# Kernel optimization log

Measured on AMD Instinct MI355X. Metric: run time of the kernel, lower is better.

The kernel has to match this reference:

```python
import jax, jax.numpy as jnp
import numpy as np

B, T, D_MODEL = 2, 2048, 2048
N_HEADS, N_KV = 16, 8
HEAD_DIM = D_MODEL // N_HEADS  # 128
EPS = 1e-6


def rmsnorm(x, g):
    # qwen-compatible: compute in fp32, scale by learned weight
    xf = x.astype(jnp.float32)
    var = jnp.mean(xf * xf, axis=-1, keepdims=True)
    return (xf * jax.lax.rsqrt(var + EPS) * g).astype(x.dtype)


def apply_rope(x, cos, sin):
    # x: [b, h, t, d]; cos/sin: [t, d]
    d = x.shape[-1]
    x1, x2 = x[..., : d // 2], x[..., d // 2 :]
    rotated = jnp.concatenate([-x2, x1], axis=-1)
    return x * cos[None, None, :, :] + rotated * sin[None, None, :, :]


def setup_inputs() -> dict:
    key = jax.random.key(0)
    ks = jax.random.split(key, 8)
    x = jax.random.normal(ks[0], (B, T, D_MODEL), dtype=jnp.float32)
    # causal mask: True = masked out
    mask = jnp.triu(jnp.ones((T, T), dtype=bool), k=1)
    # rope tables
    inv_freq = 1.0 / (1e6 ** (np.arange(0, HEAD_DIM, 2, dtype=np.float32) / HEAD_DIM))
    angles = np.arange(T, dtype=np.float32)[:, None] * inv_freq[None, :]  # [T, d/2]
    angles = np.concatenate([angles, angles], axis=1)  # [T, d]
    cos = jnp.asarray(np.cos(angles), dtype=jnp.float32)
    sin = jnp.asarray(np.sin(angles), dtype=jnp.float32)
    s = 0.02
    Wq = jax.random.normal(ks[1], (D_MODEL, D_MODEL), dtype=jnp.float32) * s
    Wk = jax.random.normal(ks[2], (N_KV * HEAD_DIM, D_MODEL), dtype=jnp.float32) * s
    Wv = jax.random.normal(ks[3], (N_KV * HEAD_DIM, D_MODEL), dtype=jnp.float32) * s
    Wo = jax.random.normal(ks[4], (D_MODEL, D_MODEL), dtype=jnp.float32) * s
    bo = jnp.zeros((D_MODEL,), dtype=jnp.float32)
    gq = jnp.ones((HEAD_DIM,), dtype=jnp.float32)
    gk = jnp.ones((HEAD_DIM,), dtype=jnp.float32)
    return {"x": x, "mask": mask, "cos": cos, "sin": sin, "Wq": Wq, "Wk": Wk,
            "Wv": Wv, "Wo": Wo, "bo": bo, "gq": gq, "gk": gk}


def reference(x, mask, cos, sin, Wq, Wk, Wv, Wo, bo, gq, gk):
    b, t, _ = x.shape
    # projections
    q = (x @ Wq.T).reshape(b, t, N_HEADS, HEAD_DIM)
    q = rmsnorm(q, gq).transpose(0, 2, 1, 3)          # [b, H, t, d]
    q = apply_rope(q, cos[:t], sin[:t])
    k = (x @ Wk.T).reshape(b, t, N_KV, HEAD_DIM)
    k = rmsnorm(k, gk).transpose(0, 2, 1, 3)          # [b, G, t, d]
    k = apply_rope(k, cos[:t], sin[:t])
    v = (x @ Wv.T).reshape(b, t, N_KV, HEAD_DIM).transpose(0, 2, 1, 3)
    # GQA broadcast of KV heads
    rep = N_HEADS // N_KV
    k = jnp.repeat(k, rep, axis=1)                    # [b, H, t, d]
    v = jnp.repeat(v, rep, axis=1)
    scores = jnp.einsum("bhqd,bhkd->bhqk", q, k)
    scores = jnp.where(mask[:t, :t][None, None], -jnp.inf, scores)
    attn = jax.nn.softmax(scores / jnp.sqrt(jnp.float32(HEAD_DIM)), axis=-1)
    out = jnp.einsum("bhqk,bhkd->bqhd", attn, v).reshape(b, t, N_HEADS * HEAD_DIM)
    return out @ Wo.T + bo
```

## Files before the change

### kernel.cpp

```cpp
#include <hip/hip_runtime.h>
#include <stdint.h>

#define B_ 2
#define T_ 2048
#define DM 2048
#define NH 16
#define NKV 8
#define HD 128
#define NQKV 4096
#define SCALE_ 0.08838834764831845f
#define SC2_ 0.12753102765f

typedef float fx4 __attribute__((ext_vector_type(4)));
typedef __bf16 bfx8 __attribute__((ext_vector_type(8)));
typedef unsigned short u16;
typedef unsigned int u32;

typedef __attribute__((address_space(1))) const void gas_t;
typedef __attribute__((address_space(3))) void las_t;

__device__ __forceinline__ u16 f2bf(float f) {
  u32 u = __float_as_uint(f);
  u = (u + 0x7fffu + ((u >> 16) & 1u)) >> 16;
  return (u16)u;
}

__device__ __forceinline__ void stage16(const void* g, void* l) {
  __builtin_amdgcn_global_load_lds((gas_t*)(uintptr_t)g, (las_t*)(uintptr_t)l,
                                   16, 0, 0);
}

__global__ void k_cvt(const float* __restrict__ in, u16* __restrict__ out, int n) {
  int i = (blockIdx.x * blockDim.x + threadIdx.x) * 4;
  if (i + 3 < n) {
    float4 v = *(const float4*)(in + i);
    u32 w0 = (u32)f2bf(v.x) | ((u32)f2bf(v.y) << 16);
    u32 w1 = (u32)f2bf(v.z) | ((u32)f2bf(v.w) << 16);
    *(uint2*)(out + i) = make_uint2(w0, w1);
  }
}

template <bool OUT_F32>
__global__ __launch_bounds__(256, 2) void k_gemm(const u16* __restrict__ A,
                                                 const u16* __restrict__ Bm,
                                                 void* __restrict__ Cv,
                                                 const float* __restrict__ bias,
                                                 int M, int N, int K) {
  __shared__ __align__(16) u16 As[128 * 32];
  __shared__ __align__(16) u16 Bs[128 * 32];
  const int nbn = N >> 7;
  const int bm = blockIdx.x / nbn, bn = blockIdx.x % nbn;
  const int tid = threadIdx.x;
  const int w = tid >> 6, lane = tid & 63;
  const int wr = w >> 1, wc = w & 1;
  const int lr = lane & 15, lg = lane >> 4;
  const u16* Ab = A + (size_t)bm * 128 * K;
  const u16* Bb = Bm + (size_t)bn * 128 * K;
  const int srow = lane >> 2, skc = (lane & 3) * 8;

  fx4 zero4 = {0.f, 0.f, 0.f, 0.f};
  fx4 acc[4][4];
#pragma unroll
  for (int m = 0; m < 4; m++)
#pragma unroll
    for (int n = 0; n < 4; n++) acc[m][n] = zero4;

  for (int k0 = 0; k0 < K; k0 += 32) {
#pragma unroll
    for (int t = 0; t < 2; t++) {
      int s = w + t * 4;
      stage16(Ab + (size_t)(s * 16 + srow) * K + k0 + skc, As + s * 512 + lane * 8);
      stage16(Bb + (size_t)(s * 16 + srow) * K + k0 + skc, Bs + s * 512 + lane * 8);
    }
    __syncthreads();
    bfx8 af[4], bfr[4];
#pragma unroll
    for (int m = 0; m < 4; m++)
      af[m] = *(const bfx8*)(As + (wr * 64 + m * 16 + lr) * 32 + lg * 8);
#pragma unroll
    for (int n = 0; n < 4; n++)
      bfr[n] = *(const bfx8*)(Bs + (wc * 64 + n * 16 + lr) * 32 + lg * 8);
#pragma unroll
    for (int m = 0; m < 4; m++)
#pragma unroll
      for (int n = 0; n < 4; n++)
        acc[m][n] = __builtin_amdgcn_mfma_f32_16x16x32_bf16(af[m], bfr[n], acc[m][n], 0, 0, 0);
    __syncthreads();
  }

  const int r0 = bm * 128 + wr * 64, c0 = bn * 128 + wc * 64;
#pragma unroll
  for (int m = 0; m < 4; m++) {
#pragma unroll
    for (int n = 0; n < 4; n++) {
      int c = c0 + n * 16 + lr;
#pragma unroll
      for (int i = 0; i < 4; i++) {
        int r = r0 + m * 16 + lg * 4 + i;
        if (OUT_F32) {
          ((float*)Cv)[(size_t)r * N + c] = acc[m][n][i] + bias[c];
        } else {
          ((u16*)Cv)[(size_t)r * N + c] = f2bf(acc[m][n][i]);
        }
      }
    }
  }
}

__global__ __launch_bounds__(256) void k_qkpost(const u16* __restrict__ qkv,
                                                const float* __restrict__ cosp,
                                                const float* __restrict__ sinp,
                                                const float* __restrict__ gq,
                                                const float* __restrict__ gk,
                                                u16* __restrict__ Qo,
                                                u16* __restrict__ Ko) {
  int bi = blockIdx.x;
  int hh = bi % 24;
  int t64 = (bi / 24) % 32;
  int b = bi / 768;
  int tid = threadIdx.x;
  int j = tid >> 2, p = tid & 3;
  int t = t64 * 64 + j;
  bool isq = hh < 16;
  int colbase = isq ? hh * 128 : 2048 + (hh - 16) * 128;
  const u16* src = qkv + ((size_t)(b * T_ + t)) * NQKV + colbase + p * 32;

  float xv[32];
#pragma unroll
  for (int c = 0; c < 4; c++) {
    uint4 raw = *(const uint4*)(src + c * 8);
    u32 wd[4] = {raw.x, raw.y, raw.z, raw.w};
#pragma unroll
    for (int q2 = 0; q2 < 4; q2++) {
      xv[c * 8 + q2 * 2 + 0] = __uint_as_float(wd[q2] << 16);
      xv[c * 8 + q2 * 2 + 1] = __uint_as_float(wd[q2] & 0xffff0000u);
    }
  }
  float ss = 0.f;
#pragma unroll
  for (int i = 0; i < 32; i++) ss += xv[i] * xv[i];
  ss += __shfl_xor(ss, 1);
  ss += __shfl_xor(ss, 2);
  float rinv = rsqrtf(ss * (1.0f / 128.0f) + 1e-6f);
  const float* g = isq ? gq : gk;
  const float* cr = cosp + (size_t)t * 128 + p * 32;
  const float* sr = sinp + (size_t)t * 128 + p * 32;

  float ov[32];
#pragma unroll
  for (int i = 0; i < 32; i++) {
    float y = xv[i] * rinv * g[p * 32 + i];
    float oth = __shfl_xor(y, 2);
    float rot = (p < 2) ? -oth : oth;
    ov[i] = y * cr[i] + rot * sr[i];
  }

  uint4 pk[4];
#pragma unroll
  for (int c = 0; c < 4; c++) {
    u32 wd[4];
#pragma unroll
    for (int q2 = 0; q2 < 4; q2++)
      wd[q2] = (u32)f2bf(ov[c * 8 + q2 * 2]) | ((u32)f2bf(ov[c * 8 + q2 * 2 + 1]) << 16);
    pk[c] = make_uint4(wd[0], wd[1], wd[2], wd[3]);
  }

  if (isq) {
    u16* dst = Qo + (((size_t)(b * NH + hh)) * T_ + t) * HD + p * 32;
#pragma unroll
    for (int c = 0; c < 4; c++) *(uint4*)(dst + c * 8) = pk[c];
  } else {
    int hk = hh - 16;
    u16* dstrow = Ko + (((size_t)(b * NKV + hk)) * T_ + t) * HD;
#pragma unroll
    for (int c = 0; c < 4; c++) {
      int C = p * 4 + c;
      int Cs = C ^ (t & 7);
      *(uint4*)(dstrow + Cs * 8) = pk[c];
    }
  }
}

__global__ __launch_bounds__(256) void k_vtr(const u16* __restrict__ qkv,
                                             u16* __restrict__ vt) {
  __shared__ __align__(16) u16 sm[128 * 64];
  int bi = blockIdx.x;
  int hv = bi & 7;
  int t64 = (bi >> 3) & 31;
  int b = bi >> 8;
  int tid = threadIdx.x;
#pragma unroll
  for (int it = 0; it < 4; it++) {
    int idx = tid + it * 256;
    int tok = idx >> 4, c = idx & 15;
    uint4 raw = *(const uint4*)(qkv + ((size_t)(b * T_ + t64 * 64 + tok)) * NQKV +
                                3072 + hv * 128 + c * 8);
    u32 wd[4] = {raw.x, raw.y, raw.z, raw.w};
#pragma unroll
    for (int q2 = 0; q2 < 4; q2++) {
      sm[(c * 8 + q2 * 2 + 0) * 64 + tok] = (u16)(wd[q2] & 0xffffu);
      sm[(c * 8 + q2 * 2 + 1) * 64 + tok] = (u16)(wd[q2] >> 16);
    }
  }
  __syncthreads();
  int d = tid >> 1, half = tid & 1;
  size_t rowb = (((size_t)(b * NKV + hv)) * HD + d) * T_ + t64 * 64;
#pragma unroll
  for (int c = 0; c < 4; c++) {
    int cg = half * 4 + c;
    int cs = cg ^ (d & 7);
    u32 wd[4];
#pragma unroll
    for (int q2 = 0; q2 < 4; q2++) {
      u32 lo = sm[d * 64 + half * 32 + c * 8 + 2 * q2];
      u32 hi = sm[d * 64 + half * 32 + c * 8 + 2 * q2 + 1];
      wd[q2] = lo | (hi << 16);
    }
    *(uint4*)(vt + rowb + cs * 8) = make_uint4(wd[0], wd[1], wd[2], wd[3]);
  }
}

__global__ __launch_bounds__(256, 2) void k_attn(const u16* __restrict__ Qg,
                                                 const u16* __restrict__ Kg,
                                                 const u16* __restrict__ Vg,
                                                 u16* __restrict__ Og) {
  __shared__ __align__(16) u16 Ks[2][64 * 128];
  __shared__ __align__(16) u16 Vs[2][128 * 64];
  __shared__ __align__(16) u16 Ps[4][16 * 64];
  const int bi = blockIdx.x;
  const int z = bi & 15, h = (bi >> 4) & 15, b = bi >> 8;
  const int hkv = h >> 1;
  const int tid = threadIdx.x, w = tid >> 6, lane = tid & 63;
  const int lr = lane & 15, lg = lane >> 4;
  const u16* kb = Kg + ((size_t)(b * NKV + hkv)) * T_ * HD;
  const u16* vb = Vg + ((size_t)(b * NKV + hkv)) * HD * T_;
  u16* pw = &Ps[w][0];
  const fx4 zero4 = {0.f, 0.f, 0.f, 0.f};

  int cur = 0;
  auto stageKV = [&](int buf, int kv0) {
    u16* Kd = &Ks[buf][0];
    u16* Vd = &Vs[buf][0];
#pragma unroll
    for (int it = 0; it < 4; it++) {
      int r = it * 16 + (tid >> 4);
      stage16(kb + (size_t)(kv0 + r) * HD + (tid & 15) * 8, Kd + it * 2048 + tid * 8);
      int d = it * 32 + (tid >> 3);
      stage16(vb + (size_t)d * T_ + kv0 + (tid & 7) * 8, Vd + it * 2048 + tid * 8);
    }
  };

#pragma unroll 1
  for (int hf = 0; hf < 2; hf++) {
    const int zt = hf ? (31 - z) : z;
    const int qr0 = zt * 64 + w * 16;
    const u16* qbase = Qg + (((size_t)(b * NH + h)) * T_ + qr0 + lr) * HD;
    bfx8 qf[4];
#pragma unroll
    for (int kk = 0; kk < 4; kk++) qf[kk] = *(const bfx8*)(qbase + kk * 32 + lg * 8);

    fx4 o[8];
#pragma unroll
    for (int nf = 0; nf < 8; nf++) o[nf] = zero4;
    float m_i[4] = {-1e30f, -1e30f, -1e30f, -1e30f};
    float l_i[4] = {0.f, 0.f, 0.f, 0.f};
    const int nch = zt + 1;

    stageKV(cur, 0);
    __syncthreads();

#pragma unroll 1
    for (int ch = 0; ch < nch; ch++) {
      if (ch + 1 < nch) stageKV(cur ^ 1, (ch + 1) * 64);
      const u16* Kd = &Ks[cur][0];
      const u16* Vd = &Vs[cur][0];
      const int kv0 = ch * 64;

      fx4 sa[4];
#pragma unroll
      for (int n = 0; n < 4; n++) sa[n] = zero4;
      __builtin_amdgcn_s_setprio(1);
#pragma unroll
      for (int n = 0; n < 4; n++) {
        const int kvl = n * 16 + lr;
        const u16* krow = Kd + kvl * 128;
#pragma unroll
        for (int kk = 0; kk < 4; kk++) {
          int cs = (kk * 4 + lg) ^ (kvl & 7);
          bfx8 kf = *(const bfx8*)(krow + cs * 8);
          sa[n] = __builtin_amdgcn_mfma_f32_16x16x32_bf16(qf[kk], kf, sa[n], 0, 0, 0);
        }
      }
      __builtin_amdgcn_s_setprio(0);

      float pv[4][4];
      if (ch == zt) {
#pragma unroll
        for (int n = 0; n < 4; n++) {
          int kcol = kv0 + n * 16 + lr;
#pragma unroll
          for (int i = 0; i < 4; i++) {
            int r = qr0 + 4 * lg + i;
            pv[n][i] = (kcol > r) ? -1e30f : sa[n][i] * SC2_;
          }
        }
      } else {
#pragma unroll
        for (int n = 0; n < 4; n++)
#pragma unroll
          for (int i = 0; i < 4; i++) pv[n][i] = sa[n][i] * SC2_;
      }

      float mx[4];
      bool need = false;
#pragma unroll
      for (int i = 0; i < 4; i++) {
        float m = fmaxf(fmaxf(pv[0][i], pv[1][i]), fmaxf(pv[2][i], pv[3][i]));
        m = fmaxf(m, __shfl_xor(m, 1));
        m = fmaxf(m, __shfl_xor(m, 2));
        m = fmaxf(m, __shfl_xor(m, 4));
        m = fmaxf(m, __shfl_xor(m, 8));
        mx[i] = m;
        need = need || (m > m_i[i] + 8.0f);
      }
      if (__any(need)) {
#pragma unroll
        for (int i = 0; i < 4; i++) {
          float mn = fmaxf(m_i[i], mx[i]);
          float f = exp2f(m_i[i] - mn);
          m_i[i] = mn;
          l_i[i] *= f;
#pragma unroll
          for (int nf = 0; nf < 8; nf++) o[nf][i] *= f;
        }
      }

#pragma unroll
      for (int i = 0; i < 4; i++) {
        int q = 4 * lg + i;
        u16* prow = pw + q * 64;
#pragma unroll
        for (int n = 0; n < 4; n++) {
          float p = exp2f(pv[n][i] - m_i[i]);
          l_i[i] += p;
          int chn = ((n * 2 + (lr >> 3)) ^ (q & 7));
          prow[chn * 8 + (lr & 7)] = f2bf(p);
        }
      }
      asm volatile("s_waitcnt lgkmcnt(0)" ::: "memory");

      bfx8 pa[2];
#pragma unroll
      for (int ks = 0; ks < 2; ks++) {
        int cp = (4 * ks + lg) ^ (lr & 7);
        pa[ks] = *(const bfx8*)(pw + lr * 64 + cp * 8);
      }
      __builtin_amdgcn_s_setprio(1);
#pragma unroll
      for (int nf = 0; nf < 8; nf++) {
        int d = nf * 16 + lr;
        const u16* vrow = Vd + d * 64;
#pragma unroll
        for (int ks = 0; ks < 2; ks++) {
          int cv = (4 * ks + lg) ^ (d & 7);
          bfx8 vf = *(const bfx8*)(vrow + cv * 8);
          o[nf] = __builtin_amdgcn_mfma_f32_16x16x32_bf16(pa[ks], vf, o[nf], 0, 0, 0);
        }
      }
      __builtin_amdgcn_s_setprio(0);
      __syncthreads();
      cur ^= 1;
    }

    float inv[4];
#pragma unroll
    for (int i = 0; i < 4; i++) {
      float l = l_i[i];
      l += __shfl_xor(l, 1);
      l += __shfl_xor(l, 2);
      l += __shfl_xor(l, 4);
      l += __shfl_xor(l, 8);
      inv[i] = 1.0f / l;
    }
    u16* ob = Og + ((size_t)(b * T_ + qr0)) * DM + h * HD;
#pragma unroll
    for (int nf = 0; nf < 8; nf++)
#pragma unroll
      for (int i = 0; i < 4; i++)
        ob[(size_t)(4 * lg + i) * DM + nf * 16 + lr] = f2bf(o[nf][i] * inv[i]);
  }
}

extern "C" void kernel_launch(void* const* d_in, const int* in_sizes, int n_in,
                              void* d_out, int out_size, void* d_ws, size_t ws_size,
                              hipStream_t stream) {
  const float* x = (const float*)d_in[0];
  const float* cosp = (const float*)d_in[2];
  const float* sinp = (const float*)d_in[3];
  const float* Wq = (const float*)d_in[4];
  const float* Wk = (const float*)d_in[5];
  const float* Wv = (const float*)d_in[6];
  const float* Wo = (const float*)d_in[7];
  const float* bo = (const float*)d_in[8];
  const float* gq = (const float*)d_in[9];
  const float* gk = (const float*)d_in[10];

  char* ws = (char*)d_ws;
  u16* xbf  = (u16*)(ws + 0);
  u16* wqkv = (u16*)(ws + 16777216);
  u16* wo   = (u16*)(ws + 33554432);
  u16* qkv  = (u16*)(ws + 41943040);
  u16* qb   = (u16*)(ws + 75497472);
  u16* kb   = (u16*)(ws + 92274688);
  u16* vt   = (u16*)(ws + 100663296);
  u16* ab   = (u16*)(ws + 109051904);
  float* out = (float*)d_out;

  k_cvt<<<8192, 256, 0, stream>>>(x, xbf, 8388608);
  k_cvt<<<4096, 256, 0, stream>>>(Wq, wqkv, 4194304);
  k_cvt<<<2048, 256, 0, stream>>>(Wk, wqkv + 4194304, 2097152);
  k_cvt<<<2048, 256, 0, stream>>>(Wv, wqkv + 6291456, 2097152);
  k_cvt<<<4096, 256, 0, stream>>>(Wo, wo, 4194304);

  k_gemm<false><<<1024, 256, 0, stream>>>(xbf, wqkv, qkv, nullptr, 4096, 4096, 2048);
  k_qkpost<<<1536, 256, 0, stream>>>(qkv, cosp, sinp, gq, gk, qb, kb);
  k_vtr<<<512, 256, 0, stream>>>(qkv, vt);
  k_attn<<<512, 256, 0, stream>>>(qb, kb, vt, ab);
  k_gemm<true><<<512, 256, 0, stream>>>(ab, wo, out, bo, 4096, 2048, 2048);
}
```

Before: 274.6 us.

## Add 256x256-tile pipelined GEMM for the QKV projection

Adds a new bf16 GEMM kernel with 256x256 output tiles, 512 threads, a double-buffered split-K LDS pipeline fed by direct global-to-LDS loads, swizzled LDS layout and raised wave priority around MFMA bursts. It replaces the 128x128 GEMM used for the fused QKV projection. The larger tile is meant to raise data reuse per loaded byte, and the interleaved staging to hide load latency. In exchange the grid drops to 256 blocks, roughly one per CU, and register pressure is high.

```diff
diff --git a/kernel.cpp b/kernel.cpp
--- a/kernel.cpp
+++ b/kernel.cpp
@@ -37,6 +37,142 @@
     u32 w0 = (u32)f2bf(v.x) | ((u32)f2bf(v.y) << 16);
     u32 w1 = (u32)f2bf(v.z) | ((u32)f2bf(v.w) << 16);
     *(uint2*)(out + i) = make_uint2(w0, w1);
+  }
+}
+
+__global__ __launch_bounds__(512, 2) void k_gemm256(const u16* __restrict__ A,
+                                                    const u16* __restrict__ Bm,
+                                                    u16* __restrict__ C,
+                                                    int M, int N, int K) {
+  __shared__ __align__(16) u16 As[2][2][256 * 32];
+  __shared__ __align__(16) u16 Bs[2][2][256 * 32];
+  const int nbn = N >> 8;
+  const int bm = blockIdx.x / nbn, bn = blockIdx.x % nbn;
+  const int tid = threadIdx.x;
+  const int w = tid >> 6, lane = tid & 63;
+  const int wm = w >> 2, wn = w & 3;
+  const int lr = lane & 15, lg = lane >> 4;
+  const int cw = (lg ^ ((lr >> 1) & 3)) * 8;
+  const u16* Ab = A + (size_t)bm * 256 * K;
+  const u16* Bb = Bm + (size_t)bn * 256 * K;
+  const int NT = K >> 6;
+
+  auto stage = [&](const u16* gb, u16* region, int tile, int kh) {
+#pragma unroll
+    for (int i = 0; i < 2; i++) {
+      int q = tid + i * 512;
+      int row = q >> 2, ch = q & 3;
+      int sc = ch ^ ((row >> 1) & 3);
+      stage16(gb + (size_t)row * K + tile * 64 + kh * 32 + sc * 8, region + q * 8);
+    }
+  };
+
+  fx4 acc[8][4];
+  const fx4 zero4 = {0.f, 0.f, 0.f, 0.f};
+#pragma unroll
+  for (int m = 0; m < 8; m++)
+#pragma unroll
+    for (int n = 0; n < 4; n++) acc[m][n] = zero4;
+
+  stage(Ab, &As[0][0][0], 0, 0);
+  stage(Bb, &Bs[0][0][0], 0, 0);
+  stage(Ab, &As[0][1][0], 0, 1);
+  stage(Bb, &Bs[0][1][0], 0, 1);
+  stage(Ab, &As[1][0][0], 1, 0);
+  stage(Bb, &Bs[1][0][0], 1, 0);
+  asm volatile("s_waitcnt vmcnt(4)" ::: "memory");
+  __builtin_amdgcn_s_barrier();
+
+  const int arow = (wm * 128 + lr) * 32;
+  const int brow = (wn * 64 + lr) * 32;
+  bfx8 af[4], bf[4];
+
+#pragma unroll 1
+  for (int t = 0; t < NT; t++) {
+    const u16* A0 = &As[t & 1][0][0];
+    const u16* A1 = &As[t & 1][1][0];
+    const u16* B0 = &Bs[t & 1][0][0];
+    const u16* B1 = &Bs[t & 1][1][0];
+    const int p1 = (t + 1) & 1, p2 = t & 1;
+
+#pragma unroll
+    for (int mi = 0; mi < 4; mi++) af[mi] = *(const bfx8*)(A0 + arow + mi * 512 + cw);
+#pragma unroll
+    for (int n = 0; n < 4; n++) bf[n] = *(const bfx8*)(B0 + brow + n * 512 + cw);
+    if (t + 1 < NT) stage(Ab, &As[p1][1][0], t + 1, 1);
+    __builtin_amdgcn_s_barrier();
+    asm volatile("s_waitcnt lgkmcnt(0)" ::: "memory");
+    __builtin_amdgcn_sched_barrier(0);
+    __builtin_amdgcn_s_setprio(1);
+#pragma unroll
+    for (int mi = 0; mi < 4; mi++)
+#pragma unroll
+      for (int n = 0; n < 4; n++)
+        acc[mi][n] = __builtin_amdgcn_mfma_f32_16x16x32_bf16(af[mi], bf[n], acc[mi][n], 0, 0, 0);
+    __builtin_amdgcn_s_setprio(0);
+    __builtin_amdgcn_s_barrier();
+
+#pragma unroll
+    for (int mi = 0; mi < 4; mi++)
+      af[mi] = *(const bfx8*)(A0 + arow + 2048 + mi * 512 + cw);
+    if (t + 1 < NT) stage(Bb, &Bs[p1][1][0], t + 1, 1);
+    __builtin_amdgcn_s_barrier();
+    asm volatile("s_waitcnt lgkmcnt(0)" ::: "memory");
+    __builtin_amdgcn_sched_barrier(0);
+    __builtin_amdgcn_s_setprio(1);
+#pragma unroll
+    for (int mi = 0; mi < 4; mi++)
+#pragma unroll
+      for (int n = 0; n < 4; n++)
+        acc[4 + mi][n] = __builtin_amdgcn_mfma_f32_16x16x32_bf16(af[mi], bf[n], acc[4 + mi][n], 0, 0, 0);
+    __builtin_amdgcn_s_setprio(0);
+    __builtin_amdgcn_s_barrier();
+
+#pragma unroll
+    for (int mi = 0; mi < 4; mi++) af[mi] = *(const bfx8*)(A1 + arow + mi * 512 + cw);
+#pragma unroll
+    for (int n = 0; n < 4; n++) bf[n] = *(const bfx8*)(B1 + brow + n * 512 + cw);
+    if (t + 2 < NT) stage(Ab, &As[p2][0][0], t + 2, 0);
+    __builtin_amdgcn_s_barrier();
+    asm volatile("s_waitcnt lgkmcnt(0)" ::: "memory");
+    __builtin_amdgcn_sched_barrier(0);
+    __builtin_amdgcn_s_setprio(1);
+#pragma unroll
+    for (int mi = 0; mi < 4; mi++)
+#pragma unroll
+      for (int n = 0; n < 4; n++)
+        acc[mi][n] = __builtin_amdgcn_mfma_f32_16x16x32_bf16(af[mi], bf[n], acc[mi][n], 0, 0, 0);
+    __builtin_amdgcn_s_setprio(0);
+    __builtin_amdgcn_s_barrier();
+
+#pragma unroll
+    for (int mi = 0; mi < 4; mi++)
+      af[mi] = *(const bfx8*)(A1 + arow + 2048 + mi * 512 + cw);
+    if (t + 2 < NT) stage(Bb, &Bs[p2][0][0], t + 2, 0);
+    __builtin_amdgcn_s_barrier();
+    asm volatile("s_waitcnt lgkmcnt(0)" ::: "memory");
+    __builtin_amdgcn_sched_barrier(0);
+    __builtin_amdgcn_s_setprio(1);
+#pragma unroll
+    for (int mi = 0; mi < 4; mi++)
+#pragma unroll
+      for (int n = 0; n < 4; n++)
+        acc[4 + mi][n] = __builtin_amdgcn_mfma_f32_16x16x32_bf16(af[mi], bf[n], acc[4 + mi][n], 0, 0, 0);
+    __builtin_amdgcn_s_setprio(0);
+    asm volatile("s_waitcnt vmcnt(4)" ::: "memory");
+    __builtin_amdgcn_s_barrier();
+  }
+
+  const int r0 = bm * 256 + wm * 128, c0 = bn * 256 + wn * 64;
+#pragma unroll
+  for (int m = 0; m < 8; m++) {
+#pragma unroll
+    for (int n = 0; n < 4; n++) {
+      int c = c0 + n * 16 + lr;
+#pragma unroll
+      for (int i = 0; i < 4; i++)
+        C[(size_t)(r0 + m * 16 + lg * 4 + i) * N + c] = f2bf(acc[m][n][i]);
+    }
   }
 }
 
@@ -422,7 +558,7 @@
   k_cvt<<<2048, 256, 0, stream>>>(Wv, wqkv + 6291456, 2097152);
   k_cvt<<<4096, 256, 0, stream>>>(Wo, wo, 4194304);
 
-  k_gemm<false><<<1024, 256, 0, stream>>>(xbf, wqkv, qkv, nullptr, 4096, 4096, 2048);
+  k_gemm256<<<256, 512, 0, stream>>>(xbf, wqkv, qkv, 4096, 4096, 2048);
   k_qkpost<<<1536, 256, 0, stream>>>(qkv, cosp, sinp, gq, gk, qb, kb);
   k_vtr<<<512, 256, 0, stream>>>(qkv, vt);
   k_attn<<<512, 256, 0, stream>>>(qb, kb, vt, ab);
```

Measured after the change: 262.0 us. -4.6%, faster.
